# Performance work log

Measured on AMD Instinct MI355X. Metric: run time of the kernel, lower is better.

The kernel has to match this reference:

```python
import jax, jax.numpy as jnp
import numpy as np

N_EMB = 1024
HEAD_SIZE = 128

def setup_inputs() -> dict:
    key = jax.random.key(0)
    kx, kq, kk, kv = jax.random.split(key, 4)
    s = 1.0 / np.sqrt(N_EMB)
    return {
        "x": jax.random.normal(kx, (4, 4096, N_EMB), dtype=jnp.float32),
        "Wq": jax.random.normal(kq, (N_EMB, HEAD_SIZE), dtype=jnp.float32) * s,
        "Wk": jax.random.normal(kk, (N_EMB, HEAD_SIZE), dtype=jnp.float32) * s,
        "Wv": jax.random.normal(kv, (N_EMB, HEAD_SIZE), dtype=jnp.float32) * s,
    }

def reference(x, Wq, Wk, Wv) -> jnp.ndarray:
    B, T, C = x.shape
    q = jnp.einsum('btc,cd->btd', x, Wq)  # [B,T,H]
    k = jnp.einsum('btc,cd->btd', x, Wk)
    v = jnp.einsum('btc,cd->btd', x, Wv)
    # NOTE: original scales by sqrt(n_emb), not sqrt(head_size)
    wei = jnp.einsum('btd,bsd->bts', q, k) / jnp.sqrt(jnp.asarray(C, x.dtype))
    causal = jnp.tril(jnp.ones((T, T), dtype=bool))
    wei = jnp.where(causal, wei, -jnp.inf)
    wei = jax.nn.softmax(wei, axis=-1)
    return jnp.einsum('bts,bsd->btd', wei, v)
```

## Files before the change

kernel.cpp:

```cpp
#include <hip/hip_runtime.h>
#include <hip/hip_bf16.h>


#define TSEQ 4096
#define NBATCH 4
#define CEMB 1024
#define HS 128
#define NWORK 272

typedef float  f32x4  __attribute__((ext_vector_type(4)));
typedef float  f32x16 __attribute__((ext_vector_type(16)));
typedef __bf16 bf16x4 __attribute__((ext_vector_type(4)));
typedef __bf16 bf16x8 __attribute__((ext_vector_type(8)));
typedef int    i32x2  __attribute__((ext_vector_type(2)));
typedef int    i32x4  __attribute__((ext_vector_type(4)));

__device__ __forceinline__ __bf16 f2b(float f) { return (__bf16)f; }
__device__ __forceinline__ float fexp2(float f) { return __builtin_amdgcn_exp2f(f); }

__device__ __forceinline__ void gl_lds16(const void* g, void* l) {
  __builtin_amdgcn_global_load_lds(
      (__attribute__((address_space(1))) void*)(g),
      (__attribute__((address_space(3))) void*)(l), 16, 0, 0);
}

__global__ void wtrans_kernel(const float* __restrict__ Wq,
                              const float* __restrict__ Wk,
                              const float* __restrict__ Wv,
                              __bf16* __restrict__ Wt) {
  const float* W = (blockIdx.y == 0) ? Wq : (blockIdx.y == 1) ? Wk : Wv;
  int g  = blockIdx.x * 256 + threadIdx.x;
  int n  = g & 127;
  int k0 = (g >> 7) * 8;
  bf16x8 v;
#pragma unroll
  for (int i = 0; i < 8; ++i) v[i] = f2b(W[(size_t)(k0 + i) * HS + n]);
  *(bf16x8*)(Wt + (size_t)blockIdx.y * HS * CEMB + (size_t)n * CEMB + k0) = v;
}

__global__ __launch_bounds__(256)
void proj_kernel(const float* __restrict__ x, const __bf16* __restrict__ Wt,
                 __bf16* __restrict__ qb, __bf16* __restrict__ kb,
                 __bf16* __restrict__ vt) {
  __shared__ __align__(16) __bf16 As[128 * 64];
  __shared__ __align__(16) __bf16 Bs[64 * 64];

  const int tid  = threadIdx.x;
  const int lane = tid & 63;
  const int w    = tid >> 6;
  const int l31  = lane & 31;
  const int half = lane >> 5;

  const int bid   = blockIdx.x;
  const int xcd   = bid & 7;
  const int rest  = bid >> 3;
  const int sub   = rest % 6;
  const int mat   = sub >> 1;
  const int nh    = sub & 1;
  const int mslab = rest / 6;
  const int m0    = (xcd + 8 * mslab) * 128;
  const int n0    = nh * 64;
  const __bf16* Wm = Wt + (size_t)mat * HS * CEMB + (size_t)n0 * CEMB;

  f32x16 acc[2];
#pragma unroll
  for (int nt = 0; nt < 2; ++nt)
#pragma unroll
    for (int r = 0; r < 16; ++r) acc[nt][r] = 0.f;

  const int ar = tid >> 3, au = tid & 7;

  for (int ks = 0; ks < CEMB; ks += 64) {
    __syncthreads();
#pragma unroll
    for (int i = 0; i < 2; ++i) {
      int c = i * 4 + w;
      int r = 8 * c + (lane >> 3);
      int u = (lane & 7) ^ (r & 7);
      gl_lds16(Wm + (size_t)r * CEMB + ks + u * 8, &Bs[c * 512]);
    }
#pragma unroll
    for (int j = 0; j < 4; ++j) {
      int r = 32 * j + ar;
      const float* p = x + (size_t)(m0 + r) * CEMB + ks + au * 8;
      f32x4 a = *(const f32x4*)p;
      f32x4 b = *(const f32x4*)(p + 4);
      bf16x8 h;
#pragma unroll
      for (int i = 0; i < 4; ++i) { h[i] = f2b(a[i]); h[4 + i] = f2b(b[i]); }
      *(bf16x8*)(As + r * 64 + (au ^ (r & 7)) * 8) = h;
    }
    __syncthreads();
#pragma unroll
    for (int kc = 0; kc < 4; ++kc) {
      int am = 32 * w + l31;
      int ua = (2 * kc + half);
      bf16x8 af = *(const bf16x8*)(As + am * 64 + (ua ^ (am & 7)) * 8);
#pragma unroll
      for (int nt = 0; nt < 2; ++nt) {
        int bn = nt * 32 + l31;
        bf16x8 bf = *(const bf16x8*)(Bs + bn * 64 + (ua ^ (bn & 7)) * 8);
        acc[nt] = __builtin_amdgcn_mfma_f32_32x32x16_bf16(af, bf, acc[nt], 0, 0, 0);
      }
    }
  }

  const float qscale = 1.4426950408889634f / 32.0f;
  if (mat == 0) {
#pragma unroll
    for (int nt = 0; nt < 2; ++nt) {
      int n = n0 + nt * 32 + l31;
#pragma unroll
      for (int r = 0; r < 16; ++r) {
        int m = m0 + 32 * w + (r & 3) + 8 * (r >> 2) + 4 * half;
        qb[(size_t)m * HS + n] = f2b(acc[nt][r] * qscale);
      }
    }
  } else if (mat == 1) {
#pragma unroll
    for (int nt = 0; nt < 2; ++nt) {
      int n = n0 + nt * 32 + l31;
#pragma unroll
      for (int r = 0; r < 16; ++r) {
        int m = m0 + 32 * w + (r & 3) + 8 * (r >> 2) + 4 * half;
        kb[(size_t)m * HS + n] = f2b(acc[nt][r]);
      }
    }
  } else {
    const int bt = m0 >> 12;
#pragma unroll
    for (int nt = 0; nt < 2; ++nt) {
      int n = n0 + nt * 32 + l31;
#pragma unroll
      for (int g = 0; g < 4; ++g) {
        bf16x4 pk;
#pragma unroll
        for (int d = 0; d < 4; ++d) pk[d] = f2b(acc[nt][4 * g + d]);
        int tl = ((m0 + 32 * w) & 4095) + 8 * g + 4 * half;
        *(bf16x4*)(vt + ((size_t)bt * HS + n) * TSEQ + tl) = pk;
      }
    }
  }
}

__global__ __launch_bounds__(256)
void attn_kernel(const __bf16* __restrict__ qb, const __bf16* __restrict__ kb,
                 const __bf16* __restrict__ vt,
                 __bf16* __restrict__ Opart, float* __restrict__ Lpart) {
  __shared__ __align__(16) __bf16 Kt[64 * 128];
  __shared__ __align__(16) __bf16 Vtl[128 * 64];

  const int tid   = threadIdx.x;
  const int lane  = tid & 63;
  const int w     = tid >> 6;
  const int l31   = lane & 31;
  const int half  = lane >> 5;
  const int batch = blockIdx.y;
  const int xw    = blockIdx.x;

  int q = 0;
  while (q < 31 && xw >= (((q + 2) * (q + 2)) >> 2)) ++q;
  const int split = xw - (((q + 1) * (q + 1)) >> 2);
  const int ntile = 2 * (q + 1);
  const int nsp   = (q + 2) >> 1;
  const int tps   = (ntile + nsp - 1) / nsp;
  const int it0   = split * tps;
  const int it1   = min(it0 + tps, ntile);

  const int strip0 = q * 128 + w * 32;
  const size_t bbase = (size_t)batch * TSEQ;

  bf16x8 qf[8];
  {
    const __bf16* qr = qb + (bbase + strip0 + l31) * HS + half * 8;
#pragma unroll
    for (int kc = 0; kc < 8; ++kc) qf[kc] = *(const bf16x8*)(qr + kc * 16);
  }

  f32x16 o[4];
#pragma unroll
  for (int nt = 0; nt < 4; ++nt)
#pragma unroll
    for (int r = 0; r < 16; ++r) o[nt][r] = 0.f;
  float lsum = 0.f;

  for (int it = it0; it < it1; ++it) {
    const int c0 = it * 64;
    __syncthreads();
#pragma unroll
    for (int i = 0; i < 4; ++i) {
      int ck = i * 4 + w;
      {
        int r  = 4 * ck + (lane >> 4);
        int u1 = lane & 15;
        int u  = (u1 & 8) | ((u1 & 7) ^ (r & 7));
        gl_lds16(kb + (bbase + c0 + r) * HS + u * 8, &Kt[ck * 512]);
      }
      {
        int d  = 8 * ck + (lane >> 3);
        int u1 = lane & 7;
        int u  = u1 ^ (d & 7);
        gl_lds16(vt + ((size_t)batch * HS + d) * TSEQ + c0 + u * 8, &Vtl[ck * 512]);
      }
    }
    __syncthreads();

    if (c0 <= strip0 + 31) {
      i32x2 pkt[2][4];
#pragma unroll
      for (int t = 0; t < 2; ++t)
#pragma unroll
        for (int j = 0; j < 4; ++j) pkt[t][j] = (i32x2){0, 0};

#pragma unroll
      for (int t = 0; t < 2; ++t) {
        if (c0 + t * 32 <= strip0 + 31) {
          f32x16 s;
#pragma unroll
          for (int r = 0; r < 16; ++r) s[r] = 0.f;
#pragma unroll
          for (int kc = 0; kc < 8; ++kc) {
            int u  = 2 * kc + half;
            int up = (u & 8) | ((u & 7) ^ (l31 & 7));
            bf16x8 kf = *(const bf16x8*)(&Kt[(t * 32 + l31) * 128 + up * 8]);
            s = __builtin_amdgcn_mfma_f32_32x32x16_bf16(kf, qf[kc], s, 0, 0, 0);
          }
          if (c0 + t * 32 + 31 > strip0) {
#pragma unroll
            for (int r = 0; r < 16; ++r) {
              int key = c0 + t * 32 + (r & 3) + 8 * (r >> 2) + 4 * half;
              if (key > strip0 + l31) s[r] = -INFINITY;
            }
          }
          float p[16], ps = 0.f;
#pragma unroll
          for (int r = 0; r < 16; ++r) { p[r] = fexp2(s[r]); ps += p[r]; }
          lsum += ps;
#pragma unroll
          for (int j = 0; j < 4; ++j) {
            bf16x4 t4;
#pragma unroll
            for (int d = 0; d < 4; ++d) t4[d] = f2b(p[4 * j + d]);
            pkt[t][j] = __builtin_bit_cast(i32x2, t4);
          }
        }
      }
#pragma unroll
      for (int kk = 0; kk < 4; ++kk) {
        int t = kk >> 1, lo = (kk & 1) * 2;
        i32x2 a = pkt[t][lo], b = pkt[t][lo + 1];
        i32x2 ra, rb;
        ra.x = __shfl_xor(a.x, 32); ra.y = __shfl_xor(a.y, 32);
        rb.x = __shfl_xor(b.x, 32); rb.y = __shfl_xor(b.y, 32);
        i32x4 af4;
        af4.x = half ? rb.x : a.x;
        af4.y = half ? rb.y : a.y;
        af4.z = half ? b.x  : ra.x;
        af4.w = half ? b.y  : ra.y;
        bf16x8 af = __builtin_bit_cast(bf16x8, af4);
#pragma unroll
        for (int nt = 0; nt < 4; ++nt) {
          int up = (2 * kk + half) ^ (l31 & 7);
          bf16x8 vf = *(const bf16x8*)(&Vtl[(nt * 32 + l31) * 64 + up * 8]);
          o[nt] = __builtin_amdgcn_mfma_f32_32x32x16_bf16(af, vf, o[nt], 0, 0, 0);
        }
      }
    }
  }

  const size_t widx = (size_t)batch * NWORK + xw;
  __bf16* Op = Opart + widx * (128 * 128);
#pragma unroll
  for (int r = 0; r < 16; ++r) {
    int rloc = w * 32 + 4 * half + (r & 3) + 8 * (r >> 2);
#pragma unroll
    for (int nt = 0; nt < 4; ++nt)
      Op[rloc * 128 + nt * 32 + l31] = f2b(o[nt][r]);
  }
  lsum += __shfl_xor(lsum, 32);
  if (half == 0) Lpart[widx * 128 + w * 32 + l31] = lsum;
}

__global__ __launch_bounds__(256)
void reduce_kernel(const __bf16* __restrict__ Opart, const float* __restrict__ Lpart,
                   float* __restrict__ out) {
  const int batch = blockIdx.y;
  const int rowg  = blockIdx.x * 8 + (threadIdx.x >> 5);
  const int q = rowg >> 7;
  const int nsp = (q + 2) >> 1;
  const int off = ((q + 1) * (q + 1)) >> 2;
  const size_t wbase = (size_t)batch * NWORK + off;
  const int row128 = rowg & 127;
  const int c0 = (threadIdx.x & 31) * 4;

  float l = 0.f;
  for (int s = 0; s < nsp; ++s) l += Lpart[(wbase + s) * 128 + row128];
  const float inv = 1.0f / l;

  const __bf16* op = Opart + wbase * (128 * 128) + row128 * 128 + c0;
  f32x4 a = {0.f, 0.f, 0.f, 0.f};
  for (int s = 0; s < nsp; ++s) {
    bf16x4 v = *(const bf16x4*)(op + (size_t)s * 128 * 128);
#pragma unroll
    for (int j = 0; j < 4; ++j) a[j] += (float)v[j];
  }
  a *= inv;
  *(f32x4*)(out + ((size_t)batch * TSEQ + rowg) * HS + c0) = a;
}

extern "C" void kernel_launch(void* const* d_in, const int* in_sizes, int n_in,
                              void* d_out, int out_size, void* d_ws, size_t ws_size,
                              hipStream_t stream) {
  const float* x  = (const float*)d_in[0];
  const float* Wq = (const float*)d_in[1];
  const float* Wk = (const float*)d_in[2];
  const float* Wv = (const float*)d_in[3];
  float* out = (float*)d_out;

  char* ws = (char*)d_ws;
  __bf16* Wt = (__bf16*)ws;
  __bf16* qb = (__bf16*)(ws + 786432);
  __bf16* kb = (__bf16*)(ws + 786432 + 4194304);
  __bf16* vt = (__bf16*)(ws + 786432 + 2 * 4194304);
  __bf16* Opart = (__bf16*)(ws + 786432 + 3 * 4194304);
  float*  Lpart = (float*)(ws + 786432 + 3 * 4194304 +
                           (size_t)NBATCH * NWORK * 128 * 128 * 2);

  wtrans_kernel<<<dim3(64, 3), 256, 0, stream>>>(Wq, Wk, Wv, Wt);
  proj_kernel<<<dim3(768), 256, 0, stream>>>(x, Wt, qb, kb, vt);
  attn_kernel<<<dim3(NWORK, NBATCH), 256, 0, stream>>>(qb, kb, vt, Opart, Lpart);
  reduce_kernel<<<dim3(512, NBATCH), 256, 0, stream>>>(Opart, Lpart, out);
}
```

Before: 173.9 us.

## Split attention into fixed 128-key work items with atomic fp32 accumulation

Attention work is re-split so each block handles exactly two 64-key tiles (528 items per batch instead of 272 variable-length ones). Partial outputs and row sums are atomically added straight into the fp32 output and a sum buffer, so the reduce pass becomes a simple normalisation and the bf16 partial buffers go away. LDS staging in both the projection and attention kernels drops the async global-to-LDS loads and XOR swizzle in favour of plain vector loads into padded rows, and the projection K-step grows to 128. The aims are better load balance and less partial-result traffic, at the cost of many fp32 atomics on the output, two extra memsets, and non-deterministic summation order.

```diff
diff --git a/kernel.cpp b/kernel.cpp
--- a/kernel.cpp
+++ b/kernel.cpp
@@ -6,7 +6,7 @@
 #define NBATCH 4
 #define CEMB 1024
 #define HS 128
-#define NWORK 272
+#define NWORK 528
 
 typedef float  f32x4  __attribute__((ext_vector_type(4)));
 typedef float  f32x16 __attribute__((ext_vector_type(16)));
@@ -17,12 +17,6 @@
 
 __device__ __forceinline__ __bf16 f2b(float f) { return (__bf16)f; }
 __device__ __forceinline__ float fexp2(float f) { return __builtin_amdgcn_exp2f(f); }
-
-__device__ __forceinline__ void gl_lds16(const void* g, void* l) {
-  __builtin_amdgcn_global_load_lds(
-      (__attribute__((address_space(1))) void*)(g),
-      (__attribute__((address_space(3))) void*)(l), 16, 0, 0);
-}
 
 __global__ void wtrans_kernel(const float* __restrict__ Wq,
                               const float* __restrict__ Wk,
@@ -42,8 +36,8 @@
 void proj_kernel(const float* __restrict__ x, const __bf16* __restrict__ Wt,
                  __bf16* __restrict__ qb, __bf16* __restrict__ kb,
                  __bf16* __restrict__ vt) {
-  __shared__ __align__(16) __bf16 As[128 * 64];
-  __shared__ __align__(16) __bf16 Bs[64 * 64];
+  __shared__ __align__(16) __bf16 As[128 * 136];
+  __shared__ __align__(16) __bf16 Bs[64 * 136];
 
   const int tid  = threadIdx.x;
   const int lane = tid & 63;
@@ -68,38 +62,35 @@
 #pragma unroll
     for (int r = 0; r < 16; ++r) acc[nt][r] = 0.f;
 
-  const int ar = tid >> 3, au = tid & 7;
-
-  for (int ks = 0; ks < CEMB; ks += 64) {
+  const int srow = tid >> 4;
+  const int soff = tid & 15;
+
+  for (int ks = 0; ks < CEMB; ks += 128) {
     __syncthreads();
 #pragma unroll
-    for (int i = 0; i < 2; ++i) {
-      int c = i * 4 + w;
-      int r = 8 * c + (lane >> 3);
-      int u = (lane & 7) ^ (r & 7);
-      gl_lds16(Wm + (size_t)r * CEMB + ks + u * 8, &Bs[c * 512]);
-    }
-#pragma unroll
-    for (int j = 0; j < 4; ++j) {
-      int r = 32 * j + ar;
-      const float* p = x + (size_t)(m0 + r) * CEMB + ks + au * 8;
+    for (int i = 0; i < 4; ++i) {
+      int r = srow + 16 * i;
+      bf16x8 v = *(const bf16x8*)(Wm + (size_t)r * CEMB + ks + soff * 8);
+      *(bf16x8*)(Bs + r * 136 + soff * 8) = v;
+    }
+#pragma unroll
+    for (int i = 0; i < 8; ++i) {
+      int r = srow + 16 * i;
+      const float* p = x + (size_t)(m0 + r) * CEMB + ks + soff * 8;
       f32x4 a = *(const f32x4*)p;
       f32x4 b = *(const f32x4*)(p + 4);
       bf16x8 h;
 #pragma unroll
-      for (int i = 0; i < 4; ++i) { h[i] = f2b(a[i]); h[4 + i] = f2b(b[i]); }
-      *(bf16x8*)(As + r * 64 + (au ^ (r & 7)) * 8) = h;
+      for (int j = 0; j < 4; ++j) { h[j] = f2b(a[j]); h[4 + j] = f2b(b[j]); }
+      *(bf16x8*)(As + r * 136 + soff * 8) = h;
     }
     __syncthreads();
 #pragma unroll
-    for (int kc = 0; kc < 4; ++kc) {
-      int am = 32 * w + l31;
-      int ua = (2 * kc + half);
-      bf16x8 af = *(const bf16x8*)(As + am * 64 + (ua ^ (am & 7)) * 8);
+    for (int kc = 0; kc < 8; ++kc) {
+      bf16x8 af = *(const bf16x8*)(As + (32 * w + l31) * 136 + kc * 16 + half * 8);
 #pragma unroll
       for (int nt = 0; nt < 2; ++nt) {
-        int bn = nt * 32 + l31;
-        bf16x8 bf = *(const bf16x8*)(Bs + bn * 64 + (ua ^ (bn & 7)) * 8);
+        bf16x8 bf = *(const bf16x8*)(Bs + (nt * 32 + l31) * 136 + kc * 16 + half * 8);
         acc[nt] = __builtin_amdgcn_mfma_f32_32x32x16_bf16(af, bf, acc[nt], 0, 0, 0);
       }
     }
@@ -146,9 +137,9 @@
 __global__ __launch_bounds__(256)
 void attn_kernel(const __bf16* __restrict__ qb, const __bf16* __restrict__ kb,
                  const __bf16* __restrict__ vt,
-                 __bf16* __restrict__ Opart, float* __restrict__ Lpart) {
-  __shared__ __align__(16) __bf16 Kt[64 * 128];
-  __shared__ __align__(16) __bf16 Vtl[128 * 64];
+                 float* __restrict__ out, float* __restrict__ Lacc) {
+  __shared__ __align__(16) __bf16 Kt[64 * 136];
+  __shared__ __align__(16) __bf16 Vtl[128 * 72];
 
   const int tid   = threadIdx.x;
   const int lane  = tid & 63;
@@ -159,13 +150,9 @@
   const int xw    = blockIdx.x;
 
   int q = 0;
-  while (q < 31 && xw >= (((q + 2) * (q + 2)) >> 2)) ++q;
-  const int split = xw - (((q + 1) * (q + 1)) >> 2);
-  const int ntile = 2 * (q + 1);
-  const int nsp   = (q + 2) >> 1;
-  const int tps   = (ntile + nsp - 1) / nsp;
-  const int it0   = split * tps;
-  const int it1   = min(it0 + tps, ntile);
+  while (q < 31 && xw >= (((q + 1) * (q + 2)) >> 1)) ++q;
+  const int split = xw - ((q * (q + 1)) >> 1);
+  const int it0   = 2 * split;
 
   const int strip0 = q * 128 + w * 32;
   const size_t bbase = (size_t)batch * TSEQ;
@@ -184,23 +171,27 @@
     for (int r = 0; r < 16; ++r) o[nt][r] = 0.f;
   float lsum = 0.f;
 
-  for (int it = it0; it < it1; ++it) {
+#pragma unroll
+  for (int ii = 0; ii < 2; ++ii) {
+    const int it = it0 + ii;
     const int c0 = it * 64;
     __syncthreads();
-#pragma unroll
-    for (int i = 0; i < 4; ++i) {
-      int ck = i * 4 + w;
-      {
-        int r  = 4 * ck + (lane >> 4);
-        int u1 = lane & 15;
-        int u  = (u1 & 8) | ((u1 & 7) ^ (r & 7));
-        gl_lds16(kb + (bbase + c0 + r) * HS + u * 8, &Kt[ck * 512]);
-      }
-      {
-        int d  = 8 * ck + (lane >> 3);
-        int u1 = lane & 7;
-        int u  = u1 ^ (d & 7);
-        gl_lds16(vt + ((size_t)batch * HS + d) * TSEQ + c0 + u * 8, &Vtl[ck * 512]);
+    {
+      const __bf16* src = kb + (bbase + c0) * HS;
+#pragma unroll
+      for (int i = 0; i < 4; ++i) {
+        int c = tid + i * 256;
+        int row = c >> 4, off = c & 15;
+        *(bf16x8*)(&Kt[row * 136 + off * 8]) =
+            *(const bf16x8*)(src + row * HS + off * 8);
+      }
+      const __bf16* vsrc = vt + (size_t)batch * HS * TSEQ + c0;
+#pragma unroll
+      for (int i = 0; i < 4; ++i) {
+        int c = tid + i * 256;
+        int n = c >> 3, off = c & 7;
+        *(bf16x8*)(&Vtl[n * 72 + off * 8]) =
+            *(const bf16x8*)(vsrc + (size_t)n * TSEQ + off * 8);
       }
     }
     __syncthreads();
@@ -220,9 +211,7 @@
           for (int r = 0; r < 16; ++r) s[r] = 0.f;
 #pragma unroll
           for (int kc = 0; kc < 8; ++kc) {
-            int u  = 2 * kc + half;
-            int up = (u & 8) | ((u & 7) ^ (l31 & 7));
-            bf16x8 kf = *(const bf16x8*)(&Kt[(t * 32 + l31) * 128 + up * 8]);
+            bf16x8 kf = *(const bf16x8*)(&Kt[(t * 32 + l31) * 136 + kc * 16 + half * 8]);
             s = __builtin_amdgcn_mfma_f32_32x32x16_bf16(kf, qf[kc], s, 0, 0, 0);
           }
           if (c0 + t * 32 + 31 > strip0) {
@@ -260,52 +249,35 @@
         bf16x8 af = __builtin_bit_cast(bf16x8, af4);
 #pragma unroll
         for (int nt = 0; nt < 4; ++nt) {
-          int up = (2 * kk + half) ^ (l31 & 7);
-          bf16x8 vf = *(const bf16x8*)(&Vtl[(nt * 32 + l31) * 64 + up * 8]);
+          bf16x8 vf = *(const bf16x8*)(&Vtl[(nt * 32 + l31) * 72 + kk * 16 + half * 8]);
           o[nt] = __builtin_amdgcn_mfma_f32_32x32x16_bf16(af, vf, o[nt], 0, 0, 0);
         }
       }
     }
   }
 
-  const size_t widx = (size_t)batch * NWORK + xw;
-  __bf16* Op = Opart + widx * (128 * 128);
+  float* Ob = out + bbase * HS;
 #pragma unroll
   for (int r = 0; r < 16; ++r) {
-    int rloc = w * 32 + 4 * half + (r & 3) + 8 * (r >> 2);
+    int rloc = strip0 + 4 * half + (r & 3) + 8 * (r >> 2);
 #pragma unroll
     for (int nt = 0; nt < 4; ++nt)
-      Op[rloc * 128 + nt * 32 + l31] = f2b(o[nt][r]);
+      atomicAdd(&Ob[(size_t)rloc * HS + nt * 32 + l31], o[nt][r]);
   }
   lsum += __shfl_xor(lsum, 32);
-  if (half == 0) Lpart[widx * 128 + w * 32 + l31] = lsum;
+  if (half == 0) atomicAdd(&Lacc[bbase + strip0 + l31], lsum);
 }
 
 __global__ __launch_bounds__(256)
-void reduce_kernel(const __bf16* __restrict__ Opart, const float* __restrict__ Lpart,
-                   float* __restrict__ out) {
+void norm_kernel(float* __restrict__ out, const float* __restrict__ Lacc) {
   const int batch = blockIdx.y;
   const int rowg  = blockIdx.x * 8 + (threadIdx.x >> 5);
-  const int q = rowg >> 7;
-  const int nsp = (q + 2) >> 1;
-  const int off = ((q + 1) * (q + 1)) >> 2;
-  const size_t wbase = (size_t)batch * NWORK + off;
-  const int row128 = rowg & 127;
   const int c0 = (threadIdx.x & 31) * 4;
-
-  float l = 0.f;
-  for (int s = 0; s < nsp; ++s) l += Lpart[(wbase + s) * 128 + row128];
-  const float inv = 1.0f / l;
-
-  const __bf16* op = Opart + wbase * (128 * 128) + row128 * 128 + c0;
-  f32x4 a = {0.f, 0.f, 0.f, 0.f};
-  for (int s = 0; s < nsp; ++s) {
-    bf16x4 v = *(const bf16x4*)(op + (size_t)s * 128 * 128);
-#pragma unroll
-    for (int j = 0; j < 4; ++j) a[j] += (float)v[j];
-  }
+  const float inv = 1.0f / Lacc[(size_t)batch * TSEQ + rowg];
+  f32x4* p = (f32x4*)(out + ((size_t)batch * TSEQ + rowg) * HS + c0);
+  f32x4 a = *p;
   a *= inv;
-  *(f32x4*)(out + ((size_t)batch * TSEQ + rowg) * HS + c0) = a;
+  *p = a;
 }
 
 extern "C" void kernel_launch(void* const* d_in, const int* in_sizes, int n_in,
@@ -322,12 +294,12 @@
   __bf16* qb = (__bf16*)(ws + 786432);
   __bf16* kb = (__bf16*)(ws + 786432 + 4194304);
   __bf16* vt = (__bf16*)(ws + 786432 + 2 * 4194304);
-  __bf16* Opart = (__bf16*)(ws + 786432 + 3 * 4194304);
-  float*  Lpart = (float*)(ws + 786432 + 3 * 4194304 +
-                           (size_t)NBATCH * NWORK * 128 * 128 * 2);
-
+  float*  Lacc = (float*)(ws + 786432 + 3 * 4194304);
+
+  hipMemsetAsync(d_out, 0, (size_t)out_size * 4, stream);
+  hipMemsetAsync(Lacc, 0, (size_t)NBATCH * TSEQ * 4, stream);
   wtrans_kernel<<<dim3(64, 3), 256, 0, stream>>>(Wq, Wk, Wv, Wt);
   proj_kernel<<<dim3(768), 256, 0, stream>>>(x, Wt, qb, kb, vt);
-  attn_kernel<<<dim3(NWORK, NBATCH), 256, 0, stream>>>(qb, kb, vt, Opart, Lpart);
-  reduce_kernel<<<dim3(512, NBATCH), 256, 0, stream>>>(Opart, Lpart, out);
-}
+  attn_kernel<<<dim3(NWORK, NBATCH), 256, 0, stream>>>(qb, kb, vt, out, Lacc);
+  norm_kernel<<<dim3(512, NBATCH), 256, 0, stream>>>(out, Lacc);
+}
```

Result: slower. 276.4 us (+59.0%).
